# Optimization experiments

Measured on AMD Instinct MI355X. Metric: run time of the kernel, lower is better.

## Reference

```python
import jax, jax.numpy as jnp
import numpy as np

N = 100000   # nodes (in_ch)
D = 128      # emb_ch
E = 1600000  # nonzeros in A_hat
RATE = 0.1   # dropout rate


def setup_inputs() -> dict:
    key = jax.random.key(0)
    k1, k2, k3, k4, k5, k6 = jax.random.split(key, 6)
    x = jnp.arange(N, dtype=jnp.int64) if jax.config.jax_enable_x64 else jnp.arange(N, dtype=jnp.int32)
    rows = jax.random.randint(k1, (E,), 0, N)
    cols = jax.random.randint(k2, (E,), 0, N)
    A_vals = jax.random.uniform(k3, (E,), dtype=jnp.float32)
    # xavier_uniform for [N, D]: bound = sqrt(6/(N+D))
    bound = float(np.sqrt(6.0 / (N + D)))
    emb_weight = jax.random.uniform(k4, (N, D), jnp.float32, -bound, bound)
    u1 = jax.random.uniform(k5, (N, D), dtype=jnp.float32)
    u2 = jax.random.uniform(k6, (N, D), dtype=jnp.float32)
    return {"x": x, "rows": rows, "cols": cols, "A_vals": A_vals,
            "emb_weight": emb_weight, "u1": u1, "u2": u2}


def _dropout(h, u):
    keep = (u >= RATE).astype(h.dtype)
    return h * keep / (1.0 - RATE)


def _spmm(rows, cols, vals, h):
    # out[i] = sum_{e: rows[e]==i} vals[e] * h[cols[e]]  -- COO SpMM
    msgs = vals[:, None] * h[cols]  # [E, D]
    return jax.ops.segment_sum(msgs, rows, num_segments=N)


def reference(x, rows, cols, A_vals, emb_weight, u1, u2):
    h0 = emb_weight[x]                       # embedding lookup [N, D]
    h1 = _spmm(rows, cols, A_vals, _dropout(h0, u1))
    h2 = _spmm(rows, cols, A_vals, _dropout(h1, u2))
    return (h0 + h1 + h2) / 3.0
```

## Files before the change

kernel.cpp:

```cpp
#include <hip/hip_runtime.h>
#include <hip/hip_fp16.h>

#define DD 128
#define SCAN_CHUNK 1024
#define ROWS_PER_BLK 16
#define MAX_STAGE 512

typedef float          f32x4 __attribute__((ext_vector_type(4)));
typedef unsigned int   u32x4 __attribute__((ext_vector_type(4)));
typedef unsigned int   u32x2 __attribute__((ext_vector_type(2)));
typedef unsigned short u16x8 __attribute__((ext_vector_type(8)));

struct __align__(8) Edge { int c; float v; };

__device__ __forceinline__ unsigned short f2h(float f) {
    return __half_as_ushort(__float2half(f));
}
__device__ __forceinline__ float2 up2(unsigned int u) {
    __half2 h = *reinterpret_cast<const __half2*>(&u);
    return __half22float2(h);
}

template <typename T>
__device__ __forceinline__ T ldnt(const T* p) { return __builtin_nontemporal_load(p); }
template <typename T>
__device__ __forceinline__ void stnt(T* p, T v) { __builtin_nontemporal_store(v, p); }

__global__ __launch_bounds__(256) void k_g1hist(const float* __restrict__ emb,
                                                const float* __restrict__ u1,
                                                ushort* __restrict__ g1,
                                                const int* __restrict__ rows,
                                                int* __restrict__ cnt,
                                                int* __restrict__ rank,
                                                int total8, int E) {
    int i = blockIdx.x * 256 + threadIdx.x;
    if (i < E) {
        int r = ldnt(rows + i);
        int old = atomicAdd(&cnt[r], 1);
        stnt(rank + i, old);
    }
    if (i < total8) {
        const f32x4* e4 = (const f32x4*)emb;
        const f32x4* a4 = (const f32x4*)u1;
        f32x4 hA = ldnt(e4 + 2 * (size_t)i);
        f32x4 hB = ldnt(e4 + 2 * (size_t)i + 1);
        f32x4 uA = ldnt(a4 + 2 * (size_t)i);
        f32x4 uB = ldnt(a4 + 2 * (size_t)i + 1);
        const float s = 1.0f / 0.9f;
        u16x8 g;
        g[0] = f2h((uA.x >= 0.1f) ? hA.x * s : 0.0f);
        g[1] = f2h((uA.y >= 0.1f) ? hA.y * s : 0.0f);
        g[2] = f2h((uA.z >= 0.1f) ? hA.z * s : 0.0f);
        g[3] = f2h((uA.w >= 0.1f) ? hA.w * s : 0.0f);
        g[4] = f2h((uB.x >= 0.1f) ? hB.x * s : 0.0f);
        g[5] = f2h((uB.y >= 0.1f) ? hB.y * s : 0.0f);
        g[6] = f2h((uB.z >= 0.1f) ? hB.z * s : 0.0f);
        g[7] = f2h((uB.w >= 0.1f) ? hB.w * s : 0.0f);
        ((u16x8*)g1)[i] = g;
    }
}

__global__ __launch_bounds__(256) void k_scan1(int* __restrict__ data,
                                               int* __restrict__ bsum, int n) {
    __shared__ int s[256];
    int tid = threadIdx.x;
    int base = blockIdx.x * SCAN_CHUNK + tid * 4;
    int v0 = 0, v1 = 0, v2 = 0, v3 = 0;
    if (base + 0 < n) v0 = data[base + 0];
    if (base + 1 < n) v1 = data[base + 1];
    if (base + 2 < n) v2 = data[base + 2];
    if (base + 3 < n) v3 = data[base + 3];
    int tsum = v0 + v1 + v2 + v3;
    s[tid] = tsum;
    __syncthreads();
    for (int off = 1; off < 256; off <<= 1) {
        int t = (tid >= off) ? s[tid - off] : 0;
        __syncthreads();
        s[tid] += t;
        __syncthreads();
    }
    int excl = s[tid] - tsum;
    if (tid == 255) bsum[blockIdx.x] = s[255];
    if (base + 0 < n) data[base + 0] = excl;
    if (base + 1 < n) data[base + 1] = excl + v0;
    if (base + 2 < n) data[base + 2] = excl + v0 + v1;
    if (base + 3 < n) data[base + 3] = excl + v0 + v1 + v2;
}

__global__ __launch_bounds__(256) void k_scan23(int* __restrict__ data,
                                                const int* __restrict__ bsum,
                                                int nb, int n) {
    __shared__ int s[1024];
    int tid = threadIdx.x;
    for (int i = tid; i < nb; i += 256) s[i] = bsum[i];
    __syncthreads();
    if (tid == 0) {
        int run = 0;
        for (int i = 0; i < nb; ++i) { int t = s[i]; s[i] = run; run += t; }
    }
    __syncthreads();
    int i = blockIdx.x * 256 + tid;
    if (i < n) data[i] += s[i >> 10];
}

__global__ __launch_bounds__(256) void k_scatter_prep(const int* __restrict__ rows,
                                                      const int* __restrict__ cols,
                                                      const float* __restrict__ vals,
                                                      const int* __restrict__ rowstart,
                                                      const int* __restrict__ rank,
                                                      Edge* __restrict__ ev,
                                                      const float* __restrict__ emb,
                                                      const float* __restrict__ u2,
                                                      ushort* __restrict__ emb16,
                                                      unsigned char* __restrict__ mask2,
                                                      int E, int total8) {
    int i = blockIdx.x * 256 + threadIdx.x;
    if (i < E) {
        int r = ldnt(rows + i);
        int c = ldnt(cols + i);
        float v = ldnt(vals + i);
        int rk = ldnt(rank + i);
        int pos = rowstart[r] + rk;
        u32x2 q;
        q.x = (unsigned int)c;
        q.y = __float_as_uint(v);
        ((u32x2*)ev)[pos] = q;
    }
    if (i < total8) {
        const f32x4* e4 = (const f32x4*)emb;
        const f32x4* b4 = (const f32x4*)u2;
        f32x4 hA = ldnt(e4 + 2 * (size_t)i);
        f32x4 hB = ldnt(e4 + 2 * (size_t)i + 1);
        f32x4 vA = ldnt(b4 + 2 * (size_t)i);
        f32x4 vB = ldnt(b4 + 2 * (size_t)i + 1);
        u16x8 e16;
        e16[0] = f2h(hA.x); e16[1] = f2h(hA.y); e16[2] = f2h(hA.z); e16[3] = f2h(hA.w);
        e16[4] = f2h(hB.x); e16[5] = f2h(hB.y); e16[6] = f2h(hB.z); e16[7] = f2h(hB.w);
        stnt((u16x8*)emb16 + i, e16);
        unsigned char m =
            (unsigned char)((vA.x >= 0.1f ? 1u : 0u)  | (vA.y >= 0.1f ? 2u : 0u)  |
                            (vA.z >= 0.1f ? 4u : 0u)  | (vA.w >= 0.1f ? 8u : 0u)  |
                            (vB.x >= 0.1f ? 16u : 0u) | (vB.y >= 0.1f ? 32u : 0u) |
                            (vB.z >= 0.1f ? 64u : 0u) | (vB.w >= 0.1f ? 128u : 0u));
        stnt(mask2 + i, m);
    }
}

template <int MODE>
__global__ __launch_bounds__(256) void k_gather(const int* __restrict__ rowstart,
                                                const Edge* __restrict__ ev,
                                                const ushort* __restrict__ srch,
                                                const unsigned char* __restrict__ mask2,
                                                const ushort* __restrict__ emb16,
                                                const ushort* __restrict__ p16in,
                                                ushort* __restrict__ p16out,
                                                ushort* __restrict__ g2,
                                                float* __restrict__ out,
                                                int N, int E) {
    __shared__ int s_rs[ROWS_PER_BLK + 1];
    __shared__ Edge s_ev[MAX_STAGE];

    int tid = threadIdx.x;
    int r0 = blockIdx.x * ROWS_PER_BLK;
    if (tid <= ROWS_PER_BLK) {
        int r = r0 + tid;
        s_rs[tid] = (r < N) ? rowstart[r] : E;
    }
    __syncthreads();
    int base = s_rs[0];
    int nblk = s_rs[ROWS_PER_BLK] - base;
    int nstage = nblk < MAX_STAGE ? nblk : MAX_STAGE;
    for (int i = tid; i < nstage; i += 256) {
        u32x2 q = ldnt((const u32x2*)(ev + base + i));
        Edge ed; ed.c = (int)q.x; ed.v = __uint_as_float(q.y);
        s_ev[i] = ed;
    }
    __syncthreads();

    int grp = tid >> 4;
    int lane = tid & 15;
    int row = r0 + grp;
    if (row >= N) return;
    int start = s_rs[grp] - base;
    int end = s_rs[grp + 1] - base;
    int eL = end < nstage ? end : nstage;

    const u32x4* __restrict__ s4 = (const u32x4*)srch;
    const Edge* __restrict__ evg = ev + base;
    float a0 = 0.f, a1 = 0.f, a2 = 0.f, a3 = 0.f;
    float a4 = 0.f, a5 = 0.f, a6 = 0.f, a7 = 0.f;

#define LDE(i) Edge E##i = s_ev[e + i];
#define GQ(i)  u32x4 q##i = s4[((size_t)E##i.c << 4) + lane];
#define ACC(i) { float vv = E##i.v; \
        float2 w0 = up2(q##i.x), w1 = up2(q##i.y), w2 = up2(q##i.z), w3 = up2(q##i.w); \
        a0 = fmaf(vv, w0.x, a0); a1 = fmaf(vv, w0.y, a1); \
        a2 = fmaf(vv, w1.x, a2); a3 = fmaf(vv, w1.y, a3); \
        a4 = fmaf(vv, w2.x, a4); a5 = fmaf(vv, w2.y, a5); \
        a6 = fmaf(vv, w3.x, a6); a7 = fmaf(vv, w3.y, a7); }

    int e = start;
    for (; e + 8 <= eL; e += 8) {
        LDE(0) LDE(1) LDE(2) LDE(3) LDE(4) LDE(5) LDE(6) LDE(7)
        GQ(0) GQ(1) GQ(2) GQ(3) GQ(4) GQ(5) GQ(6) GQ(7)
        ACC(0) ACC(1) ACC(2) ACC(3) ACC(4) ACC(5) ACC(6) ACC(7)
    }
    if (e + 4 <= eL) {
        LDE(0) LDE(1) LDE(2) LDE(3)
        GQ(0) GQ(1) GQ(2) GQ(3)
        ACC(0) ACC(1) ACC(2) ACC(3)
        e += 4;
    }
    for (; e < eL; ++e) {
        LDE(0) GQ(0) ACC(0)
    }
    for (; e < end; ++e) {
        Edge E0; { u32x2 q_ = ldnt((const u32x2*)(evg + e));
                   E0.c = (int)q_.x; E0.v = __uint_as_float(q_.y); }
        GQ(0) ACC(0)
    }
#undef LDE
#undef GQ
#undef ACC

    size_t o = ((size_t)row << 7) + (size_t)lane * 8;
    if (MODE == 1) {
        unsigned int m = ldnt(mask2 + (size_t)row * 16 + lane);
        const float s = 1.0f / 0.9f;
        u16x8 gg;
        gg[0] = (m & 1u)   ? f2h(a0 * s) : (ushort)0;
        gg[1] = (m & 2u)   ? f2h(a1 * s) : (ushort)0;
        gg[2] = (m & 4u)   ? f2h(a2 * s) : (ushort)0;
        gg[3] = (m & 8u)   ? f2h(a3 * s) : (ushort)0;
        gg[4] = (m & 16u)  ? f2h(a4 * s) : (ushort)0;
        gg[5] = (m & 32u)  ? f2h(a5 * s) : (ushort)0;
        gg[6] = (m & 64u)  ? f2h(a6 * s) : (ushort)0;
        gg[7] = (m & 128u) ? f2h(a7 * s) : (ushort)0;
        stnt((u16x8*)(g2 + o), gg);
        u16x8 pp;
        pp[0] = f2h(a0); pp[1] = f2h(a1); pp[2] = f2h(a2); pp[3] = f2h(a3);
        pp[4] = f2h(a4); pp[5] = f2h(a5); pp[6] = f2h(a6); pp[7] = f2h(a7);
        stnt((u16x8*)(p16out + o), pp);
    } else {
        u32x4 eq = ldnt((const u32x4*)(emb16 + o));
        u32x4 pq = ldnt((const u32x4*)(p16in + o));
        float2 e0 = up2(eq.x), e1 = up2(eq.y), e2 = up2(eq.z), e3 = up2(eq.w);
        float2 p0 = up2(pq.x), p1 = up2(pq.y), p2 = up2(pq.z), p3 = up2(pq.w);
        const float t3 = 1.0f / 3.0f;
        f32x4 rA, rB;
        rA.x = (e0.x + p0.x + a0) * t3;
        rA.y = (e0.y + p0.y + a1) * t3;
        rA.z = (e1.x + p1.x + a2) * t3;
        rA.w = (e1.y + p1.y + a3) * t3;
        rB.x = (e2.x + p2.x + a4) * t3;
        rB.y = (e2.y + p2.y + a5) * t3;
        rB.z = (e3.x + p3.x + a6) * t3;
        rB.w = (e3.y + p3.y + a7) * t3;
        stnt((f32x4*)(out + o), rA);
        stnt((f32x4*)(out + o) + 1, rB);
    }
}


extern "C" void kernel_launch(void* const* d_in, const int* in_sizes, int n_in,
                              void* d_out, int out_size, void* d_ws, size_t ws_size,
                              hipStream_t stream) {
    const int* rows = (const int*)d_in[1];
    const int* cols = (const int*)d_in[2];
    const float* vals = (const float*)d_in[3];
    const float* emb = (const float*)d_in[4];
    const float* u1 = (const float*)d_in[5];
    const float* u2 = (const float*)d_in[6];
    float* out = (float*)d_out;

    const int N = in_sizes[0];
    const int E = in_sizes[1];
    const size_t ND = (size_t)N * DD;

    char* ws = (char*)d_ws;
    Edge* ev     = (Edge*)ws;   ws += (size_t)E * sizeof(Edge);
    ushort* g1   = (ushort*)ws; ws += ND * sizeof(ushort);
    ushort* g2   = (ushort*)ws; ws += ND * sizeof(ushort);
    ushort* p16  = (ushort*)ws; ws += ND * sizeof(ushort);
    ushort* emb16= (ushort*)ws; ws += ND * sizeof(ushort);
    int* cnt     = (int*)ws;    ws += (size_t)N * sizeof(int);
    int* rank    = (int*)ws;    ws += (size_t)E * sizeof(int);
    int* bsum    = (int*)ws;    ws += 4096;
    unsigned char* mask2 = (unsigned char*)ws;

    const int total8 = (int)(ND / 8);
    const int prepBlocks = (total8 + 255) / 256;
    const int gridE = (E + 255) / 256;
    const int gridFuse = prepBlocks > gridE ? prepBlocks : gridE;
    const int nScanBlocks = (N + SCAN_CHUNK - 1) / SCAN_CHUNK;
    const int gridRow = (N + ROWS_PER_BLK - 1) / ROWS_PER_BLK;

    hipMemsetAsync(cnt, 0, (size_t)N * sizeof(int), stream);
    k_g1hist<<<gridFuse, 256, 0, stream>>>(emb, u1, g1, rows, cnt, rank, total8, E);
    k_scan1<<<nScanBlocks, 256, 0, stream>>>(cnt, bsum, N);
    k_scan23<<<(N + 255) / 256, 256, 0, stream>>>(cnt, bsum, nScanBlocks, N);
    k_scatter_prep<<<gridFuse, 256, 0, stream>>>(rows, cols, vals, cnt, rank, ev,
                                                 emb, u2, emb16, mask2, E, total8);
    k_gather<1><<<gridRow, 256, 0, stream>>>(cnt, ev, g1, mask2, nullptr, nullptr,
                                             p16, g2, nullptr, N, E);
    k_gather<2><<<gridRow, 256, 0, stream>>>(cnt, ev, g2, nullptr, emb16, p16,
                                             nullptr, nullptr, out, N, E);
}
```

Before: 411.3 us.

## Privatize row histogram into eight copies and pack ranks as 16-bit

```diff
diff --git a/kernel.cpp b/kernel.cpp
--- a/kernel.cpp
+++ b/kernel.cpp
@@ -5,6 +5,7 @@
 #define SCAN_CHUNK 1024
 #define ROWS_PER_BLK 16
 #define MAX_STAGE 512
+#define NCOPY 8
 
 typedef float          f32x4 __attribute__((ext_vector_type(4)));
 typedef unsigned int   u32x4 __attribute__((ext_vector_type(4)));
@@ -30,22 +31,29 @@
                                                 const float* __restrict__ u1,
                                                 ushort* __restrict__ g1,
                                                 const int* __restrict__ rows,
-                                                int* __restrict__ cnt,
-                                                int* __restrict__ rank,
-                                                int total8, int E) {
+                                                int* __restrict__ cnt8,
+                                                ushort* __restrict__ rank,
+                                                int total8, int E, int N) {
     int i = blockIdx.x * 256 + threadIdx.x;
-    if (i < E) {
-        int r = ldnt(rows + i);
-        int old = atomicAdd(&cnt[r], 1);
-        stnt(rank + i, old);
-    }
-    if (i < total8) {
+    bool doE = i < E;
+    bool doS = i < total8;
+    int r = 0;
+    if (doE) r = ldnt(rows + i);
+    f32x4 hA, hB, uA, uB;
+    if (doS) {
         const f32x4* e4 = (const f32x4*)emb;
         const f32x4* a4 = (const f32x4*)u1;
-        f32x4 hA = ldnt(e4 + 2 * (size_t)i);
-        f32x4 hB = ldnt(e4 + 2 * (size_t)i + 1);
-        f32x4 uA = ldnt(a4 + 2 * (size_t)i);
-        f32x4 uB = ldnt(a4 + 2 * (size_t)i + 1);
+        hA = ldnt(e4 + 2 * (size_t)i);
+        hB = ldnt(e4 + 2 * (size_t)i + 1);
+        uA = ldnt(a4 + 2 * (size_t)i);
+        uB = ldnt(a4 + 2 * (size_t)i + 1);
+    }
+    if (doE) {
+        int k = blockIdx.x & (NCOPY - 1);
+        int old = atomicAdd(&cnt8[(size_t)k * N + r], 1);
+        stnt(rank + i, (ushort)((k << 13) | old));
+    }
+    if (doS) {
         const float s = 1.0f / 0.9f;
         u16x8 g;
         g[0] = f2h((uA.x >= 0.1f) ? hA.x * s : 0.0f);
@@ -60,17 +68,31 @@
     }
 }
 
-__global__ __launch_bounds__(256) void k_scan1(int* __restrict__ data,
+__global__ __launch_bounds__(256) void k_scan1(int* __restrict__ cnt8,
+                                               int* __restrict__ rs,
                                                int* __restrict__ bsum, int n) {
     __shared__ int s[256];
     int tid = threadIdx.x;
     int base = blockIdx.x * SCAN_CHUNK + tid * 4;
-    int v0 = 0, v1 = 0, v2 = 0, v3 = 0;
-    if (base + 0 < n) v0 = data[base + 0];
-    if (base + 1 < n) v1 = data[base + 1];
-    if (base + 2 < n) v2 = data[base + 2];
-    if (base + 3 < n) v3 = data[base + 3];
-    int tsum = v0 + v1 + v2 + v3;
+    int tot[4];
+#pragma unroll
+    for (int j = 0; j < 4; ++j) {
+        int row = base + j;
+        int t = 0;
+        if (row < n) {
+            int c[NCOPY];
+#pragma unroll
+            for (int k = 0; k < NCOPY; ++k) c[k] = cnt8[(size_t)k * n + row];
+#pragma unroll
+            for (int k = 0; k < NCOPY; ++k) {
+                int cc = c[k];
+                cnt8[(size_t)k * n + row] = t;
+                t += cc;
+            }
+        }
+        tot[j] = t;
+    }
+    int tsum = tot[0] + tot[1] + tot[2] + tot[3];
     s[tid] = tsum;
     __syncthreads();
     for (int off = 1; off < 256; off <<= 1) {
@@ -81,13 +103,16 @@
     }
     int excl = s[tid] - tsum;
     if (tid == 255) bsum[blockIdx.x] = s[255];
-    if (base + 0 < n) data[base + 0] = excl;
-    if (base + 1 < n) data[base + 1] = excl + v0;
-    if (base + 2 < n) data[base + 2] = excl + v0 + v1;
-    if (base + 3 < n) data[base + 3] = excl + v0 + v1 + v2;
-}
-
-__global__ __launch_bounds__(256) void k_scan23(int* __restrict__ data,
+    int run = excl;
+#pragma unroll
+    for (int j = 0; j < 4; ++j) {
+        int row = base + j;
+        if (row < n) rs[row] = run;
+        run += tot[j];
+    }
+}
+
+__global__ __launch_bounds__(256) void k_scan23(int* __restrict__ rs,
                                                 const int* __restrict__ bsum,
                                                 int nb, int n) {
     __shared__ int s[1024];
@@ -100,39 +125,50 @@
     }
     __syncthreads();
     int i = blockIdx.x * 256 + tid;
-    if (i < n) data[i] += s[i >> 10];
+    if (i < n) rs[i] += s[i >> 10];
 }
 
 __global__ __launch_bounds__(256) void k_scatter_prep(const int* __restrict__ rows,
                                                       const int* __restrict__ cols,
                                                       const float* __restrict__ vals,
-                                                      const int* __restrict__ rowstart,
-                                                      const int* __restrict__ rank,
+                                                      const int* __restrict__ rs,
+                                                      const int* __restrict__ cnt8,
+                                                      const ushort* __restrict__ rank,
                                                       Edge* __restrict__ ev,
                                                       const float* __restrict__ emb,
                                                       const float* __restrict__ u2,
                                                       ushort* __restrict__ emb16,
                                                       unsigned char* __restrict__ mask2,
-                                                      int E, int total8) {
+                                                      int E, int total8, int N) {
     int i = blockIdx.x * 256 + threadIdx.x;
-    if (i < E) {
-        int r = ldnt(rows + i);
-        int c = ldnt(cols + i);
-        float v = ldnt(vals + i);
-        int rk = ldnt(rank + i);
-        int pos = rowstart[r] + rk;
+    bool doE = i < E;
+    bool doS = i < total8;
+    int r = 0, c = 0; float v = 0.f; unsigned int rk = 0;
+    if (doE) {
+        r = ldnt(rows + i);
+        c = ldnt(cols + i);
+        v = ldnt(vals + i);
+        rk = ldnt(rank + i);
+    }
+    f32x4 hA, hB, vA, vB;
+    if (doS) {
+        const f32x4* e4 = (const f32x4*)emb;
+        const f32x4* b4 = (const f32x4*)u2;
+        hA = ldnt(e4 + 2 * (size_t)i);
+        hB = ldnt(e4 + 2 * (size_t)i + 1);
+        vA = ldnt(b4 + 2 * (size_t)i);
+        vB = ldnt(b4 + 2 * (size_t)i + 1);
+    }
+    if (doE) {
+        int k = rk >> 13;
+        int rin = rk & 0x1FFF;
+        int pos = rs[r] + cnt8[(size_t)k * N + r] + rin;
         u32x2 q;
         q.x = (unsigned int)c;
         q.y = __float_as_uint(v);
         ((u32x2*)ev)[pos] = q;
     }
-    if (i < total8) {
-        const f32x4* e4 = (const f32x4*)emb;
-        const f32x4* b4 = (const f32x4*)u2;
-        f32x4 hA = ldnt(e4 + 2 * (size_t)i);
-        f32x4 hB = ldnt(e4 + 2 * (size_t)i + 1);
-        f32x4 vA = ldnt(b4 + 2 * (size_t)i);
-        f32x4 vB = ldnt(b4 + 2 * (size_t)i + 1);
+    if (doS) {
         u16x8 e16;
         e16[0] = f2h(hA.x); e16[1] = f2h(hA.y); e16[2] = f2h(hA.z); e16[3] = f2h(hA.w);
         e16[4] = f2h(hB.x); e16[5] = f2h(hB.y); e16[6] = f2h(hB.z); e16[7] = f2h(hB.w);
@@ -283,8 +319,9 @@
     ushort* g2   = (ushort*)ws; ws += ND * sizeof(ushort);
     ushort* p16  = (ushort*)ws; ws += ND * sizeof(ushort);
     ushort* emb16= (ushort*)ws; ws += ND * sizeof(ushort);
-    int* cnt     = (int*)ws;    ws += (size_t)N * sizeof(int);
-    int* rank    = (int*)ws;    ws += (size_t)E * sizeof(int);
+    int* cnt8    = (int*)ws;    ws += (size_t)NCOPY * N * sizeof(int);
+    int* rs      = (int*)ws;    ws += (size_t)N * sizeof(int);
+    ushort* rank = (ushort*)ws; ws += (size_t)E * sizeof(ushort);
     int* bsum    = (int*)ws;    ws += 4096;
     unsigned char* mask2 = (unsigned char*)ws;
 
@@ -295,14 +332,16 @@
     const int nScanBlocks = (N + SCAN_CHUNK - 1) / SCAN_CHUNK;
     const int gridRow = (N + ROWS_PER_BLK - 1) / ROWS_PER_BLK;
 
-    hipMemsetAsync(cnt, 0, (size_t)N * sizeof(int), stream);
-    k_g1hist<<<gridFuse, 256, 0, stream>>>(emb, u1, g1, rows, cnt, rank, total8, E);
-    k_scan1<<<nScanBlocks, 256, 0, stream>>>(cnt, bsum, N);
-    k_scan23<<<(N + 255) / 256, 256, 0, stream>>>(cnt, bsum, nScanBlocks, N);
-    k_scatter_prep<<<gridFuse, 256, 0, stream>>>(rows, cols, vals, cnt, rank, ev,
-                                                 emb, u2, emb16, mask2, E, total8);
-    k_gather<1><<<gridRow, 256, 0, stream>>>(cnt, ev, g1, mask2, nullptr, nullptr,
+    hipMemsetAsync(cnt8, 0, (size_t)NCOPY * N * sizeof(int), stream);
+    k_g1hist<<<gridFuse, 256, 0, stream>>>(emb, u1, g1, rows, cnt8, rank,
+                                           total8, E, N);
+    k_scan1<<<nScanBlocks, 256, 0, stream>>>(cnt8, rs, bsum, N);
+    k_scan23<<<(N + 255) / 256, 256, 0, stream>>>(rs, bsum, nScanBlocks, N);
+    k_scatter_prep<<<gridFuse, 256, 0, stream>>>(rows, cols, vals, rs, cnt8, rank,
+                                                 ev, emb, u2, emb16, mask2,
+                                                 E, total8, N);
+    k_gather<1><<<gridRow, 256, 0, stream>>>(rs, ev, g1, mask2, nullptr, nullptr,
                                              p16, g2, nullptr, N, E);
-    k_gather<2><<<gridRow, 256, 0, stream>>>(cnt, ev, g2, nullptr, emb16, p16,
+    k_gather<2><<<gridRow, 256, 0, stream>>>(rs, ev, g2, nullptr, emb16, p16,
                                              nullptr, nullptr, out, N, E);
 }
```

Result: no change. 419.1 us (+1.9%).
